# Performance work log

Hardware: AMD Instinct MI355X
Metric: run time of the kernel (lower is better)

The kernel has to match this reference:

```python
import jax, jax.numpy as jnp
import numpy as np
from jax.ops import segment_sum, segment_max

N = 100000   # nodes
E = 300000   # directed edges (3-regular fullerene cages)
F_IN = 16    # num_node_features
D = 128      # hidden_dim
H = 8        # heads
C = D // H   # per-head channels = 16
L = 4        # num_layers
G = 1600     # number of graphs in the batch
EPS = 1e-5   # BatchNorm eps
NEG_SLOPE = 0.2  # GATConv leaky_relu slope


def setup_inputs() -> dict:
    key = jax.random.key(0)
    ks = jax.random.split(key, 16)
    x = jax.random.normal(ks[0], (N, F_IN), jnp.float32)
    edge_index = jax.random.randint(ks[1], (2, E), 0, N, dtype=jnp.int64)
    batch = jnp.sort(jax.random.randint(ks[2], (N,), 0, G, dtype=jnp.int64))
    def w(k, shape, fan_in):
        return jax.random.normal(k, shape, jnp.float32) / np.sqrt(fan_in)
    return {
        "x": x, "edge_index": edge_index, "batch": batch,
        "Wp": w(ks[3], (F_IN, D), F_IN), "bp": jnp.zeros((D,), jnp.float32),
        "Wg": w(ks[4], (L, D, D), D),                       # per-layer GAT lin weight
        "asrc": w(ks[5], (L, H, C), C), "adst": w(ks[6], (L, H, C), C),
        "bg": jnp.zeros((L, D), jnp.float32),               # GAT bias
        "gamma": jnp.ones((L, D), jnp.float32), "beta": jnp.zeros((L, D), jnp.float32),
        "hW1": w(ks[7], (3, D, D // 2), D), "hb1": jnp.zeros((3, D // 2), jnp.float32),
        "hW2": w(ks[8], (3, D // 2, 1), D // 2), "hb2": jnp.zeros((3, 1), jnp.float32),
    }


def _gat_layer(x, W, att_src, att_dst, bias, src, dst):
    # PyG GATConv: linear transform per head, additive attention, scatter-softmax over dst
    xh = (x @ W).reshape(N, H, C)                      # [N,H,C]
    a_src = (xh * att_src).sum(-1)                     # [N,H]
    a_dst = (xh * att_dst).sum(-1)                     # [N,H]
    e = jax.nn.leaky_relu(a_src[src] + a_dst[dst], NEG_SLOPE)   # [E',H]
    m = segment_max(e, dst, num_segments=N)            # stable softmax per destination
    ex = jnp.exp(e - m[dst])
    denom = segment_sum(ex, dst, num_segments=N)       # > 0 (self-loops present)
    alpha = ex / denom[dst]                            # [E',H]
    out = segment_sum(alpha[:, :, None] * xh[src], dst, num_segments=N)  # [N,H,C]
    return out.reshape(N, D) + bias


def _forward(x, Wp, bp, Wg, asrc, adst, bg, gamma, beta, hW1, hb1, hW2, hb2,
             edge_index, batch):
    # add self loops (GATConv default add_self_loops=True)
    loop = jnp.arange(N, dtype=edge_index.dtype)
    src = jnp.concatenate([edge_index[0], loop])
    dst = jnp.concatenate([edge_index[1], loop])
    h = jax.nn.relu(x @ Wp + bp)
    for i in range(L):
        h = _gat_layer(h, Wg[i], asrc[i], adst[i], bg[i], src, dst)
        mu = h.mean(0)
        var = ((h - mu) ** 2).mean(0)                   # biased var (BN training math)
        h = (h - mu) / jnp.sqrt(var + EPS) * gamma[i] + beta[i]
        h = jax.nn.relu(h)                              # dropout off (eval)
    # global mean pool over graphs
    counts = segment_sum(jnp.ones((N,), h.dtype), batch, num_segments=G)
    pooled = segment_sum(h, batch, num_segments=G) / jnp.maximum(counts, 1.0)[:, None]
    # 3 output heads: Linear -> ReLU -> Linear(1)
    hid = jax.nn.relu(jnp.einsum('gd,kdm->kgm', pooled, hW1) + hb1[:, None, :])
    out = jnp.einsum('kgm,kmo->kgo', hid, hW2) + hb2[:, None, :]   # [3,G,1]
    return out[:, :, 0].T                               # [G,3]


def reference(x, edge_index, batch, Wp, bp, Wg, asrc, adst, bg, gamma, beta,
              hW1, hb1, hW2, hb2):
    return _forward(x, Wp, bp, Wg, asrc, adst, bg, gamma, beta,
                    hW1, hb1, hW2, hb2, edge_index, batch)
```

## Files before the change

kernel.cpp:

```cpp
#include <hip/hip_runtime.h>

#define D 128
#define NH 8
#define CH 16
#define NEG 0.2f
#define BN_EPS 1e-5f
#define MAXDEG 32
#define NSLICE 32
#define WROWS 144

typedef unsigned int uint;
typedef unsigned short ushort;
typedef __attribute__((ext_vector_type(8))) short bfrag;
typedef __attribute__((ext_vector_type(4))) float ffrag;

__device__ __forceinline__ float bf_lo(uint u){ return __uint_as_float(u << 16); }
__device__ __forceinline__ float bf_hi(uint u){ return __uint_as_float(u & 0xffff0000u); }
__device__ __forceinline__ float bf2f(ushort s){ return __uint_as_float(((uint)s) << 16); }
__device__ __forceinline__ ushort f2b(float f){
  uint u = __float_as_uint(f);
  u += 0x7fffu + ((u >> 16) & 1u);
  return (ushort)(u >> 16);
}

__global__ void k_scatter(const int* __restrict__ ei, int* __restrict__ deg,
                          int* __restrict__ col, int E){
  int e = blockIdx.x*blockDim.x + threadIdx.x;
  if (e < E){
    int d = ei[E + e];
    int pos = atomicAdd(&deg[d], 1);
    if (pos < MAXDEG) col[(size_t)d*MAXDEG + pos] = ei[e];
  }
}

__global__ void k_setup(const float* __restrict__ x, const float* __restrict__ Wp,
                        const float* __restrict__ bp, ushort* __restrict__ h,
                        const int* __restrict__ batch, int* __restrict__ gs,
                        const float* __restrict__ Wg, const float* __restrict__ asrc,
                        const float* __restrict__ adst, ushort* __restrict__ WtB,
                        int n, int G, int WTOT, int bInit, int bGb, int bWp){
  int bid = blockIdx.x;
  int t = threadIdx.x;
  if (bid < bInit){
    int i = bid*256 + t;
    if (i >= n*32) return;
    int nid = i >> 5, d4 = (i & 31)*4;
    const float* xr = x + nid*16;
    float s[4] = { bp[d4], bp[d4+1], bp[d4+2], bp[d4+3] };
#pragma unroll
    for (int k = 0; k < 16; k++){
      float xv = xr[k];
      const float* wr = Wp + k*D + d4;
      s[0] += xv*wr[0]; s[1] += xv*wr[1]; s[2] += xv*wr[2]; s[3] += xv*wr[3];
    }
    uint2 o;
    o.x = ((uint)f2b(fmaxf(s[0],0.f))) | (((uint)f2b(fmaxf(s[1],0.f))) << 16);
    o.y = ((uint)f2b(fmaxf(s[2],0.f))) | (((uint)f2b(fmaxf(s[3],0.f))) << 16);
    *(uint2*)(h + (size_t)nid*D + d4) = o;
  } else if (bid < bInit + bGb){
    int i = (bid - bInit)*256 + t;
    if (i >= n) return;
    int b = batch[i];
    int bpv = (i == 0) ? -1 : batch[i-1];
    for (int g = bpv + 1; g <= b; g++) gs[g] = i;
    if (i == n-1) for (int g = b + 1; g <= G; g++) gs[g] = n;
  } else if (bid < bInit + bGb + bWp){
    int i = (bid - bInit - bGb)*256 + t;
    if (i >= WTOT) return;
    int l = i >> 14, r = i & 16383, nn = r >> 7, kk = r & 127;
    WtB[(size_t)l*WROWS*D + nn*D + kk] = f2b(Wg[(size_t)l*16384 + kk*128 + nn]);
  } else {
    int i = (bid - bInit - bGb - bWp)*256 + t;
    int wscTot = (WTOT >> 14)*16*128;
    if (i >= wscTot) return;
    int l = i >> 11, r = i & 2047, j = r >> 7, k = r & 127;
    const float* wrow = Wg + (size_t)l*16384 + k*128;
    float s = 0.f;
    if (j < 8){
      const float* av = asrc + l*128 + j*16;
#pragma unroll
      for (int c = 0; c < 16; c++) s += wrow[j*16 + c] * av[c];
    } else {
      const float* av = adst + l*128 + (j - 8)*16;
#pragma unroll
      for (int c = 0; c < 16; c++) s += wrow[(j - 8)*16 + c] * av[c];
    }
    WtB[(size_t)l*WROWS*D + (128 + j)*D + k] = f2b(s);
  }
}

__global__ __launch_bounds__(512) void k_gemm(const ushort* __restrict__ hin,
                                              const ushort* __restrict__ WtB,
                                              ushort* __restrict__ xh,
                                              float* __restrict__ sc2,
                                              const float* __restrict__ bnsum,
                                              const float* __restrict__ gamma,
                                              const float* __restrict__ beta,
                                              int n, int first){
  __shared__ __align__(16) ushort wL[WROWS*136];
  __shared__ float sS[128], sB[128];
  int t = threadIdx.x;
  int wid = t >> 6, lane = t & 63, l15 = lane & 15, quad = lane >> 4;
  int n0 = blockIdx.x * 256;
  int rbase = wid*32;

  if (t < 128){
    float sc, sh;
    if (first){ sc = 1.f; sh = 0.f; }
    else {
      float s = 0.f, s2 = 0.f;
#pragma unroll 8
      for (int sl = 0; sl < NSLICE; sl++){
        s  += bnsum[sl*256 + t];
        s2 += bnsum[sl*256 + 128 + t];
      }
      float invn = 1.0f / (float)n;
      float mu = s * invn;
      float var = s2 * invn - mu*mu;
      sc = gamma[t] * rsqrtf(var + BN_EPS);
      sh = beta[t] - mu*sc;
    }
    sS[t] = sc; sB[t] = sh;
  }
#pragma unroll
  for (int i = 0; i < 5; i++){
    int u = t + i*512;
    if (u < WROWS*16){
      int r = u >> 4, c8 = u & 15;
      *(uint4*)(wL + r*136 + c8*8) = *(const uint4*)(WtB + (size_t)r*D + c8*8);
    }
  }
  __syncthreads();

  bfrag a[2][4];
#pragma unroll
  for (int mt = 0; mt < 2; mt++){
    int row = n0 + rbase + mt*16 + l15;
#pragma unroll
    for (int ks = 0; ks < 4; ks++){
      union { bfrag b; ushort us[8]; } in, ov;
      in.b = (bfrag){0,0,0,0,0,0,0,0};
      if (row < n) in.b = *(const bfrag*)(hin + (size_t)row*D + ks*32 + quad*8);
      int kb = ks*32 + quad*8;
#pragma unroll
      for (int j = 0; j < 8; j++){
        float f = bf2f(in.us[j])*sS[kb + j] + sB[kb + j];
        ov.us[j] = f2b(f > 0.f ? f : 0.f);
      }
      a[mt][ks] = ov.b;
    }
  }

  ffrag acc[2][9];
#pragma unroll
  for (int mt = 0; mt < 2; mt++)
#pragma unroll
    for (int nt = 0; nt < 9; nt++) acc[mt][nt] = (ffrag){0.f,0.f,0.f,0.f};

#pragma unroll
  for (int nt = 0; nt < 9; nt++){
#pragma unroll
    for (int ks = 0; ks < 4; ks++){
      bfrag b = *(const bfrag*)(wL + (nt*16 + l15)*136 + ks*32 + quad*8);
      acc[0][nt] = __builtin_amdgcn_mfma_f32_16x16x32_bf16(a[0][ks], b, acc[0][nt], 0, 0, 0);
      acc[1][nt] = __builtin_amdgcn_mfma_f32_16x16x32_bf16(a[1][ks], b, acc[1][nt], 0, 0, 0);
    }
  }

#pragma unroll
  for (int mt = 0; mt < 2; mt++)
#pragma unroll
    for (int r = 0; r < 4; r++){
      int grow = n0 + rbase + mt*16 + quad*4 + r;
      if (grow < n){
        sc2[(size_t)grow*16 + l15] = acc[mt][8][r];
        ushort* xr = xh + (size_t)grow*D + l15;
#pragma unroll
        for (int nt = 0; nt < 8; nt++)
          xr[nt*16] = f2b(acc[mt][nt][r]);
      }
    }
}

__global__ __launch_bounds__(512) void k_agg(const uint* __restrict__ xh32,
                                             const float* __restrict__ sc2,
                                             const int* __restrict__ deg,
                                             const int* __restrict__ col,
                                             const float* __restrict__ bg,
                                             ushort* __restrict__ hout,
                                             float* __restrict__ bnsum, int n){
  int wv = threadIdx.x >> 6;
  int l  = threadIdx.x & 63;
  int hs = l & 7;
  int jc = l >> 3;
  int n0 = (blockIdx.x*8 + wv)*2;
  int n1 = n0 + 1;
  bool vA = n0 < n, vB = n1 < n;
  int na = vA ? n0 : 0, nb = vB ? n1 : 0;

  float bnS0=0.f, bnS1=0.f, bnQ0=0.f, bnQ1=0.f;
  float b0 = bg[2*l], b1 = bg[2*l + 1];

  int cntA = deg[na]; if (cntA > MAXDEG) cntA = MAXDEG; if (!vA) cntA = 0;
  int cntB = deg[nb]; if (cntB > MAXDEG) cntB = MAXDEG; if (!vB) cntB = 0;
  const int* cbA = col + na*MAXDEG;
  const int* cbB = col + nb*MAXDEG;
  int idxA[8], idxB[8];
#pragma unroll
  for (int j = 0; j < 8; j++){ idxA[j] = cbA[j]; idxB[j] = cbB[j]; }
  int myA = cbA[jc], myB = cbB[jc];
  float asA = sc2[na*16 + hs],     asB = sc2[nb*16 + hs];
  float adA = sc2[na*16 + 8 + hs], adB = sc2[nb*16 + 8 + hs];
  uint selfA = xh32[na*64 + l],    selfB = xh32[nb*64 + l];
  float avA = sc2[myA*16 + hs],    avB = sc2[myB*16 + hs];
  uint gA[8], gB[8];
#pragma unroll
  for (int j = 0; j < 8; j++){ gA[j] = xh32[idxA[j]*64 + l]; gB[j] = xh32[idxB[j]*64 + l]; }

  int ccA = cntA < 8 ? cntA : 8;
  int ccB = cntB < 8 ? cntB : 8;
  float e0A = asA + adA; e0A = e0A > 0.f ? e0A : NEG*e0A;
  float e0B = asB + adB; e0B = e0B > 0.f ? e0B : NEG*e0B;
  float mA = e0A, dnmA = 1.f, accA0 = bf_lo(selfA), accA1 = bf_hi(selfA);
  float mB = e0B, dnmB = 1.f, accB0 = bf_lo(selfB), accB1 = bf_hi(selfB);

  float eA = -1e30f, eB = -1e30f;
  if (jc < ccA){ float ee = avA + adA; eA = ee > 0.f ? ee : NEG*ee; }
  if (jc < ccB){ float ee = avB + adB; eB = ee > 0.f ? ee : NEG*ee; }
  float mcA = eA, mcB = eB;
  mcA = fmaxf(mcA, __shfl_xor(mcA, 8));  mcB = fmaxf(mcB, __shfl_xor(mcB, 8));
  mcA = fmaxf(mcA, __shfl_xor(mcA, 16)); mcB = fmaxf(mcB, __shfl_xor(mcB, 16));
  mcA = fmaxf(mcA, __shfl_xor(mcA, 32)); mcB = fmaxf(mcB, __shfl_xor(mcB, 32));
  float mnA = fmaxf(mA, mcA),            mnB = fmaxf(mB, mcB);
  float rscA = __expf(mA - mnA),         rscB = __expf(mB - mnB);
  float wA = (jc < ccA) ? __expf(eA - mnA) : 0.f;
  float wB = (jc < ccB) ? __expf(eB - mnB) : 0.f;
  float wsA = wA, wsB = wB;
  wsA += __shfl_xor(wsA, 8);  wsB += __shfl_xor(wsB, 8);
  wsA += __shfl_xor(wsA, 16); wsB += __shfl_xor(wsB, 16);
  wsA += __shfl_xor(wsA, 32); wsB += __shfl_xor(wsB, 32);
  dnmA = dnmA*rscA + wsA;                dnmB = dnmB*rscB + wsB;
  mA = mnA;                              mB = mnB;
  float rcA = __shfl(rscA, jc),          rcB = __shfl(rscB, jc);
  accA0 *= rcA; accA1 *= rcA;            accB0 *= rcB; accB1 *= rcB;
#pragma unroll
  for (int jj = 0; jj < 8; jj++){
    float wjA = __shfl(wA, jj*8 + jc);
    float wjB = __shfl(wB, jj*8 + jc);
    accA0 += wjA * bf_lo(gA[jj]); accA1 += wjA * bf_hi(gA[jj]);
    accB0 += wjB * bf_lo(gB[jj]); accB1 += wjB * bf_hi(gB[jj]);
  }

  for (int c0 = 8; c0 < cntA; c0 += 8){
    int cc2 = cntA - c0; if (cc2 > 8) cc2 = 8;
    int my2 = cbA[c0 + jc];
    float av2 = sc2[my2*16 + hs];
    uint g2[8];
#pragma unroll
    for (int jj = 0; jj < 8; jj++) g2[jj] = xh32[cbA[c0 + jj]*64 + l];
    float e2 = -1e30f;
    if (jc < cc2){ float ee = av2 + adA; e2 = ee > 0.f ? ee : NEG*ee; }
    float mc2 = e2;
    mc2 = fmaxf(mc2, __shfl_xor(mc2, 8));
    mc2 = fmaxf(mc2, __shfl_xor(mc2, 16));
    mc2 = fmaxf(mc2, __shfl_xor(mc2, 32));
    float mn2 = fmaxf(mA, mc2);
    float rsc2 = __expf(mA - mn2);
    float w2 = (jc < cc2) ? __expf(e2 - mn2) : 0.f;
    float ws2 = w2;
    ws2 += __shfl_xor(ws2, 8);
    ws2 += __shfl_xor(ws2, 16);
    ws2 += __shfl_xor(ws2, 32);
    dnmA = dnmA*rsc2 + ws2; mA = mn2;
    float rc2 = __shfl(rsc2, jc);
    accA0 *= rc2; accA1 *= rc2;
#pragma unroll
    for (int jj = 0; jj < 8; jj++){
      float wj = __shfl(w2, jj*8 + jc);
      accA0 += wj * bf_lo(g2[jj]); accA1 += wj * bf_hi(g2[jj]);
    }
  }
  for (int c0 = 8; c0 < cntB; c0 += 8){
    int cc2 = cntB - c0; if (cc2 > 8) cc2 = 8;
    int my2 = cbB[c0 + jc];
    float av2 = sc2[my2*16 + hs];
    uint g2[8];
#pragma unroll
    for (int jj = 0; jj < 8; jj++) g2[jj] = xh32[cbB[c0 + jj]*64 + l];
    float e2 = -1e30f;
    if (jc < cc2){ float ee = av2 + adB; e2 = ee > 0.f ? ee : NEG*ee; }
    float mc2 = e2;
    mc2 = fmaxf(mc2, __shfl_xor(mc2, 8));
    mc2 = fmaxf(mc2, __shfl_xor(mc2, 16));
    mc2 = fmaxf(mc2, __shfl_xor(mc2, 32));
    float mn2 = fmaxf(mB, mc2);
    float rsc2 = __expf(mB - mn2);
    float w2 = (jc < cc2) ? __expf(e2 - mn2) : 0.f;
    float ws2 = w2;
    ws2 += __shfl_xor(ws2, 8);
    ws2 += __shfl_xor(ws2, 16);
    ws2 += __shfl_xor(ws2, 32);
    dnmB = dnmB*rsc2 + ws2; mB = mn2;
    float rc2 = __shfl(rsc2, jc);
    accB0 *= rc2; accB1 *= rc2;
#pragma unroll
    for (int jj = 0; jj < 8; jj++){
      float wj = __shfl(w2, jj*8 + jc);
      accB0 += wj * bf_lo(g2[jj]); accB1 += wj * bf_hi(g2[jj]);
    }
  }

  float dfA = __shfl(dnmA, jc), dfB = __shfl(dnmB, jc);
  float invA = 1.0f / dfA,      invB = 1.0f / dfB;
  float oA0 = accA0*invA + b0,  oA1 = accA1*invA + b1;
  float oB0 = accB0*invB + b0,  oB1 = accB1*invB + b1;
  if (vA){
    uint p = ((uint)f2b(oA0)) | (((uint)f2b(oA1)) << 16);
    ((uint*)hout)[n0*64 + l] = p;
    bnS0 += oA0; bnS1 += oA1; bnQ0 += oA0*oA0; bnQ1 += oA1*oA1;
  }
  if (vB){
    uint p = ((uint)f2b(oB0)) | (((uint)f2b(oB1)) << 16);
    ((uint*)hout)[n1*64 + l] = p;
    bnS0 += oB0; bnS1 += oB1; bnQ0 += oB0*oB0; bnQ1 += oB1*oB1;
  }

  __shared__ float red[8][64][4];
  red[wv][l][0] = bnS0; red[wv][l][1] = bnS1; red[wv][l][2] = bnQ0; red[wv][l][3] = bnQ1;
  __syncthreads();
  if (wv == 0){
    float t0 = 0.f, t1 = 0.f, t2 = 0.f, t3 = 0.f;
#pragma unroll
    for (int k = 0; k < 8; k++){
      t0 += red[k][l][0]; t1 += red[k][l][1];
      t2 += red[k][l][2]; t3 += red[k][l][3];
    }
    float* bs = bnsum + (blockIdx.x & (NSLICE - 1))*256;
    atomicAdd(&bs[2*l],       t0);
    atomicAdd(&bs[2*l + 1],   t1);
    atomicAdd(&bs[128 + 2*l], t2);
    atomicAdd(&bs[129 + 2*l], t3);
  }
}

__global__ __launch_bounds__(128) void k_poolheads(const ushort* __restrict__ h,
                                                   const int* __restrict__ gs,
                                                   const float* __restrict__ bnsum,
                                                   const float* __restrict__ gamma,
                                                   const float* __restrict__ beta,
                                                   const float* __restrict__ hW1,
                                                   const float* __restrict__ hb1,
                                                   const float* __restrict__ hW2,
                                                   const float* __restrict__ hb2,
                                                   float* __restrict__ out, int n){
  int g = blockIdx.x;
  int t = threadIdx.x;
  __shared__ float sp[128];
  int st = gs[g], en = gs[g + 1];
  float sm = 0.f, s2 = 0.f;
#pragma unroll 8
  for (int sl = 0; sl < NSLICE; sl++){
    sm += bnsum[sl*256 + t];
    s2 += bnsum[sl*256 + 128 + t];
  }
  float invn = 1.0f / (float)n;
  float mu = sm * invn;
  float var = s2 * invn - mu*mu;
  float sc = gamma[t] * rsqrtf(var + BN_EPS);
  float sh = beta[t] - mu*sc;
  float s = 0.f;
  for (int r = st; r < en; r++){
    float v = bf2f(h[(size_t)r*D + t]) * sc + sh;
    s += v > 0.f ? v : 0.f;
  }
  float cnt = (float)(en - st);
  sp[t] = s / fmaxf(cnt, 1.0f);
  __syncthreads();
  int wv = t >> 6, m = t & 63;
  for (int k = wv; k < 3; k += 2){
    float acc = hb1[k*64 + m];
    const float* w = hW1 + k*8192 + m;
#pragma unroll 16
    for (int d = 0; d < 128; d++) acc += sp[d] * w[d*64];
    float val = fmaxf(acc, 0.f) * hW2[k*64 + m];
#pragma unroll
    for (int off = 32; off; off >>= 1) val += __shfl_down(val, off);
    if (m == 0) out[(size_t)g*3 + k] = val + hb2[k];
  }
}

extern "C" void kernel_launch(void* const* d_in, const int* in_sizes, int n_in,
                              void* d_out, int out_size, void* d_ws, size_t ws_size,
                              hipStream_t stream){
  const float* x    = (const float*)d_in[0];
  const int*   ei   = (const int*)d_in[1];
  const int*   batch= (const int*)d_in[2];
  const float* Wp   = (const float*)d_in[3];
  const float* bp   = (const float*)d_in[4];
  const float* Wg   = (const float*)d_in[5];
  const float* asrc = (const float*)d_in[6];
  const float* adst = (const float*)d_in[7];
  const float* bg   = (const float*)d_in[8];
  const float* gamma= (const float*)d_in[9];
  const float* beta = (const float*)d_in[10];
  const float* hW1  = (const float*)d_in[11];
  const float* hb1  = (const float*)d_in[12];
  const float* hW2  = (const float*)d_in[13];
  const float* hb2  = (const float*)d_in[14];
  float* out = (float*)d_out;

  const int E = in_sizes[1] / 2;
  const int N = in_sizes[2];
  const int G = out_size / 3;
  const int WTOT = in_sizes[5];
  const int L = WTOT / 16384;

  char* w = (char*)d_ws;
  auto alloc = [&](size_t bytes){ char* p = w; w += (bytes + 255) & ~(size_t)255; return p; };
  ushort* h     = (ushort*)alloc((size_t)N*D*2);
  ushort* xh    = (ushort*)alloc((size_t)N*D*2);
  float* sc2    = (float*)alloc((size_t)N*16*4);
  int*   deg    = (int*)  alloc((size_t)N*4);
  int*   col    = (int*)  alloc(((size_t)N*MAXDEG + 64)*4);
  float* bnsumL = (float*)alloc((size_t)4*NSLICE*256*4);
  char*  zend   = w;
  int*   gs     = (int*)  alloc((size_t)(G + 1)*4);
  ushort* WtB   = (ushort*)alloc((size_t)L*WROWS*D*2);

  hipMemsetAsync(deg, 0, (size_t)(zend - (char*)deg), stream);
  k_scatter<<<(E + 255)/256, 256, 0, stream>>>(ei, deg, col, E);

  const int bInit = (N*32 + 255)/256;
  const int bGb   = (N + 255)/256;
  const int bWp   = (WTOT + 255)/256;
  const int bWsc  = (WTOT/8 + 255)/256;
  k_setup<<<bInit + bGb + bWp + bWsc, 256, 0, stream>>>(
      x, Wp, bp, h, batch, gs, Wg, asrc, adst, WtB,
      N, G, WTOT, bInit, bGb, bWp);

  for (int l = 0; l < 4; l++){
    float* bnPrev = bnsumL + (size_t)(l - 1)*NSLICE*256;
    float* bnCur  = bnsumL + (size_t)l*NSLICE*256;
    k_gemm<<<(N + 255)/256, 512, 0, stream>>>(h, WtB + (size_t)l*WROWS*D, xh, sc2,
                                              l == 0 ? bnCur : bnPrev,
                                              gamma + l*D, beta + l*D, N, l == 0);
    k_agg<<<(N + 15)/16, 512, 0, stream>>>((const uint*)xh, sc2, deg, col,
                                           bg + l*D, h, bnCur, N);
  }

  k_poolheads<<<G, 128, 0, stream>>>(h, gs, bnsumL + (size_t)3*NSLICE*256,
                                     gamma + 3*D, beta + 3*D,
                                     hW1, hb1, hW2, hb2, out, N);
}
```

Before: 384.8 us.

## Compute per-lane softmax in aggregation without shuffles; fuse edge scatter into setup

```diff
diff --git a/kernel.cpp b/kernel.cpp
--- a/kernel.cpp
+++ b/kernel.cpp
@@ -23,22 +23,15 @@
   return (ushort)(u >> 16);
 }
 
-__global__ void k_scatter(const int* __restrict__ ei, int* __restrict__ deg,
-                          int* __restrict__ col, int E){
-  int e = blockIdx.x*blockDim.x + threadIdx.x;
-  if (e < E){
-    int d = ei[E + e];
-    int pos = atomicAdd(&deg[d], 1);
-    if (pos < MAXDEG) col[(size_t)d*MAXDEG + pos] = ei[e];
-  }
-}
-
 __global__ void k_setup(const float* __restrict__ x, const float* __restrict__ Wp,
                         const float* __restrict__ bp, ushort* __restrict__ h,
                         const int* __restrict__ batch, int* __restrict__ gs,
                         const float* __restrict__ Wg, const float* __restrict__ asrc,
                         const float* __restrict__ adst, ushort* __restrict__ WtB,
-                        int n, int G, int WTOT, int bInit, int bGb, int bWp){
+                        const int* __restrict__ ei, int* __restrict__ deg,
+                        int* __restrict__ col,
+                        int n, int G, int WTOT, int E,
+                        int bInit, int bGb, int bWp, int bWsc){
   int bid = blockIdx.x;
   int t = threadIdx.x;
   if (bid < bInit){
@@ -69,7 +62,7 @@
     if (i >= WTOT) return;
     int l = i >> 14, r = i & 16383, nn = r >> 7, kk = r & 127;
     WtB[(size_t)l*WROWS*D + nn*D + kk] = f2b(Wg[(size_t)l*16384 + kk*128 + nn]);
-  } else {
+  } else if (bid < bInit + bGb + bWp + bWsc){
     int i = (bid - bInit - bGb - bWp)*256 + t;
     int wscTot = (WTOT >> 14)*16*128;
     if (i >= wscTot) return;
@@ -86,6 +79,13 @@
       for (int c = 0; c < 16; c++) s += wrow[(j - 8)*16 + c] * av[c];
     }
     WtB[(size_t)l*WROWS*D + (128 + j)*D + k] = f2b(s);
+  } else {
+    int e = (bid - bInit - bGb - bWp - bWsc)*256 + t;
+    if (e < E){
+      int d = ei[E + e];
+      int pos = atomicAdd(&deg[d], 1);
+      if (pos < MAXDEG) col[(size_t)d*MAXDEG + pos] = ei[e];
+    }
   }
 }
 
@@ -191,8 +191,7 @@
                                              float* __restrict__ bnsum, int n){
   int wv = threadIdx.x >> 6;
   int l  = threadIdx.x & 63;
-  int hs = l & 7;
-  int jc = l >> 3;
+  int hd = l >> 3;
   int n0 = (blockIdx.x*8 + wv)*2;
   int n1 = n0 + 1;
   bool vA = n0 < n, vB = n1 < n;
@@ -207,113 +206,107 @@
   const int* cbB = col + nb*MAXDEG;
   int idxA[8], idxB[8];
 #pragma unroll
-  for (int j = 0; j < 8; j++){ idxA[j] = cbA[j]; idxB[j] = cbB[j]; }
-  int myA = cbA[jc], myB = cbB[jc];
-  float asA = sc2[na*16 + hs],     asB = sc2[nb*16 + hs];
-  float adA = sc2[na*16 + 8 + hs], adB = sc2[nb*16 + 8 + hs];
+  for (int j = 0; j < 8; j++){
+    int ia = cbA[j]; idxA[j] = (j < cntA) ? ia : na;
+    int ib = cbB[j]; idxB[j] = (j < cntB) ? ib : nb;
+  }
+  float adA = sc2[na*16 + 8 + hd], adB = sc2[nb*16 + 8 + hd];
+  float asA = sc2[na*16 + hd],     asB = sc2[nb*16 + hd];
   uint selfA = xh32[na*64 + l],    selfB = xh32[nb*64 + l];
-  float avA = sc2[myA*16 + hs],    avB = sc2[myB*16 + hs];
+  float sA[8], sB_[8];
+#pragma unroll
+  for (int j = 0; j < 8; j++){ sA[j] = sc2[idxA[j]*16 + hd]; sB_[j] = sc2[idxB[j]*16 + hd]; }
   uint gA[8], gB[8];
 #pragma unroll
   for (int j = 0; j < 8; j++){ gA[j] = xh32[idxA[j]*64 + l]; gB[j] = xh32[idxB[j]*64 + l]; }
 
-  int ccA = cntA < 8 ? cntA : 8;
-  int ccB = cntB < 8 ? cntB : 8;
+  float eA[8], eB[8];
+#pragma unroll
+  for (int j = 0; j < 8; j++){
+    float ea = sA[j]  + adA; ea = ea > 0.f ? ea : NEG*ea;
+    float eb = sB_[j] + adB; eb = eb > 0.f ? eb : NEG*eb;
+    eA[j] = (j < cntA) ? ea : -1e30f;
+    eB[j] = (j < cntB) ? eb : -1e30f;
+  }
   float e0A = asA + adA; e0A = e0A > 0.f ? e0A : NEG*e0A;
   float e0B = asB + adB; e0B = e0B > 0.f ? e0B : NEG*e0B;
-  float mA = e0A, dnmA = 1.f, accA0 = bf_lo(selfA), accA1 = bf_hi(selfA);
-  float mB = e0B, dnmB = 1.f, accB0 = bf_lo(selfB), accB1 = bf_hi(selfB);
-
-  float eA = -1e30f, eB = -1e30f;
-  if (jc < ccA){ float ee = avA + adA; eA = ee > 0.f ? ee : NEG*ee; }
-  if (jc < ccB){ float ee = avB + adB; eB = ee > 0.f ? ee : NEG*ee; }
-  float mcA = eA, mcB = eB;
-  mcA = fmaxf(mcA, __shfl_xor(mcA, 8));  mcB = fmaxf(mcB, __shfl_xor(mcB, 8));
-  mcA = fmaxf(mcA, __shfl_xor(mcA, 16)); mcB = fmaxf(mcB, __shfl_xor(mcB, 16));
-  mcA = fmaxf(mcA, __shfl_xor(mcA, 32)); mcB = fmaxf(mcB, __shfl_xor(mcB, 32));
-  float mnA = fmaxf(mA, mcA),            mnB = fmaxf(mB, mcB);
-  float rscA = __expf(mA - mnA),         rscB = __expf(mB - mnB);
-  float wA = (jc < ccA) ? __expf(eA - mnA) : 0.f;
-  float wB = (jc < ccB) ? __expf(eB - mnB) : 0.f;
-  float wsA = wA, wsB = wB;
-  wsA += __shfl_xor(wsA, 8);  wsB += __shfl_xor(wsB, 8);
-  wsA += __shfl_xor(wsA, 16); wsB += __shfl_xor(wsB, 16);
-  wsA += __shfl_xor(wsA, 32); wsB += __shfl_xor(wsB, 32);
-  dnmA = dnmA*rscA + wsA;                dnmB = dnmB*rscB + wsB;
-  mA = mnA;                              mB = mnB;
-  float rcA = __shfl(rscA, jc),          rcB = __shfl(rscB, jc);
-  accA0 *= rcA; accA1 *= rcA;            accB0 *= rcB; accB1 *= rcB;
-#pragma unroll
-  for (int jj = 0; jj < 8; jj++){
-    float wjA = __shfl(wA, jj*8 + jc);
-    float wjB = __shfl(wB, jj*8 + jc);
-    accA0 += wjA * bf_lo(gA[jj]); accA1 += wjA * bf_hi(gA[jj]);
-    accB0 += wjB * bf_lo(gB[jj]); accB1 += wjB * bf_hi(gB[jj]);
+  float mA = fmaxf(fmaxf(fmaxf(eA[0],eA[1]), fmaxf(eA[2],eA[3])),
+                   fmaxf(fmaxf(eA[4],eA[5]), fmaxf(eA[6],eA[7])));
+  float mB = fmaxf(fmaxf(fmaxf(eB[0],eB[1]), fmaxf(eB[2],eB[3])),
+                   fmaxf(fmaxf(eB[4],eB[5]), fmaxf(eB[6],eB[7])));
+  mA = fmaxf(mA, e0A);
+  mB = fmaxf(mB, e0B);
+  float w0A = __expf(e0A - mA), w0B = __expf(e0B - mB);
+  float denA = w0A, denB = w0B;
+  float accA0 = w0A*bf_lo(selfA), accA1 = w0A*bf_hi(selfA);
+  float accB0 = w0B*bf_lo(selfB), accB1 = w0B*bf_hi(selfB);
+#pragma unroll
+  for (int j = 0; j < 8; j++){
+    float wa = __expf(eA[j] - mA);
+    float wb = __expf(eB[j] - mB);
+    denA += wa; denB += wb;
+    accA0 += wa*bf_lo(gA[j]); accA1 += wa*bf_hi(gA[j]);
+    accB0 += wb*bf_lo(gB[j]); accB1 += wb*bf_hi(gB[j]);
   }
 
   for (int c0 = 8; c0 < cntA; c0 += 8){
-    int cc2 = cntA - c0; if (cc2 > 8) cc2 = 8;
-    int my2 = cbA[c0 + jc];
-    float av2 = sc2[my2*16 + hs];
-    uint g2[8];
-#pragma unroll
-    for (int jj = 0; jj < 8; jj++) g2[jj] = xh32[cbA[c0 + jj]*64 + l];
-    float e2 = -1e30f;
-    if (jc < cc2){ float ee = av2 + adA; e2 = ee > 0.f ? ee : NEG*ee; }
-    float mc2 = e2;
-    mc2 = fmaxf(mc2, __shfl_xor(mc2, 8));
-    mc2 = fmaxf(mc2, __shfl_xor(mc2, 16));
-    mc2 = fmaxf(mc2, __shfl_xor(mc2, 32));
-    float mn2 = fmaxf(mA, mc2);
-    float rsc2 = __expf(mA - mn2);
-    float w2 = (jc < cc2) ? __expf(e2 - mn2) : 0.f;
-    float ws2 = w2;
-    ws2 += __shfl_xor(ws2, 8);
-    ws2 += __shfl_xor(ws2, 16);
-    ws2 += __shfl_xor(ws2, 32);
-    dnmA = dnmA*rsc2 + ws2; mA = mn2;
-    float rc2 = __shfl(rsc2, jc);
-    accA0 *= rc2; accA1 *= rc2;
-#pragma unroll
-    for (int jj = 0; jj < 8; jj++){
-      float wj = __shfl(w2, jj*8 + jc);
-      accA0 += wj * bf_lo(g2[jj]); accA1 += wj * bf_hi(g2[jj]);
-    }
+    int idx2[8];
+#pragma unroll
+    for (int j = 0; j < 8; j++){ int v = cbA[c0 + j]; idx2[j] = (c0 + j < cntA) ? v : na; }
+    float s2v[8]; uint g2[8];
+#pragma unroll
+    for (int j = 0; j < 8; j++) s2v[j] = sc2[idx2[j]*16 + hd];
+#pragma unroll
+    for (int j = 0; j < 8; j++) g2[j] = xh32[idx2[j]*64 + l];
+    float e2[8];
+#pragma unroll
+    for (int j = 0; j < 8; j++){
+      float ee = s2v[j] + adA; ee = ee > 0.f ? ee : NEG*ee;
+      e2[j] = (c0 + j < cntA) ? ee : -1e30f;
+    }
+    float m2 = fmaxf(fmaxf(fmaxf(e2[0],e2[1]), fmaxf(e2[2],e2[3])),
+                     fmaxf(fmaxf(e2[4],e2[5]), fmaxf(e2[6],e2[7])));
+    float mn = fmaxf(mA, m2);
+    float r = __expf(mA - mn);
+    denA *= r; accA0 *= r; accA1 *= r;
+#pragma unroll
+    for (int j = 0; j < 8; j++){
+      float w = __expf(e2[j] - mn);
+      denA += w; accA0 += w*bf_lo(g2[j]); accA1 += w*bf_hi(g2[j]);
+    }
+    mA = mn;
   }
   for (int c0 = 8; c0 < cntB; c0 += 8){
-    int cc2 = cntB - c0; if (cc2 > 8) cc2 = 8;
-    int my2 = cbB[c0 + jc];
-    float av2 = sc2[my2*16 + hs];
-    uint g2[8];
-#pragma unroll
-    for (int jj = 0; jj < 8; jj++) g2[jj] = xh32[cbB[c0 + jj]*64 + l];
-    float e2 = -1e30f;
-    if (jc < cc2){ float ee = av2 + adB; e2 = ee > 0.f ? ee : NEG*ee; }
-    float mc2 = e2;
-    mc2 = fmaxf(mc2, __shfl_xor(mc2, 8));
-    mc2 = fmaxf(mc2, __shfl_xor(mc2, 16));
-    mc2 = fmaxf(mc2, __shfl_xor(mc2, 32));
-    float mn2 = fmaxf(mB, mc2);
-    float rsc2 = __expf(mB - mn2);
-    float w2 = (jc < cc2) ? __expf(e2 - mn2) : 0.f;
-    float ws2 = w2;
-    ws2 += __shfl_xor(ws2, 8);
-    ws2 += __shfl_xor(ws2, 16);
-    ws2 += __shfl_xor(ws2, 32);
-    dnmB = dnmB*rsc2 + ws2; mB = mn2;
-    float rc2 = __shfl(rsc2, jc);
-    accB0 *= rc2; accB1 *= rc2;
-#pragma unroll
-    for (int jj = 0; jj < 8; jj++){
-      float wj = __shfl(w2, jj*8 + jc);
-      accB0 += wj * bf_lo(g2[jj]); accB1 += wj * bf_hi(g2[jj]);
-    }
-  }
-
-  float dfA = __shfl(dnmA, jc), dfB = __shfl(dnmB, jc);
-  float invA = 1.0f / dfA,      invB = 1.0f / dfB;
-  float oA0 = accA0*invA + b0,  oA1 = accA1*invA + b1;
-  float oB0 = accB0*invB + b0,  oB1 = accB1*invB + b1;
+    int idx2[8];
+#pragma unroll
+    for (int j = 0; j < 8; j++){ int v = cbB[c0 + j]; idx2[j] = (c0 + j < cntB) ? v : nb; }
+    float s2v[8]; uint g2[8];
+#pragma unroll
+    for (int j = 0; j < 8; j++) s2v[j] = sc2[idx2[j]*16 + hd];
+#pragma unroll
+    for (int j = 0; j < 8; j++) g2[j] = xh32[idx2[j]*64 + l];
+    float e2[8];
+#pragma unroll
+    for (int j = 0; j < 8; j++){
+      float ee = s2v[j] + adB; ee = ee > 0.f ? ee : NEG*ee;
+      e2[j] = (c0 + j < cntB) ? ee : -1e30f;
+    }
+    float m2 = fmaxf(fmaxf(fmaxf(e2[0],e2[1]), fmaxf(e2[2],e2[3])),
+                     fmaxf(fmaxf(e2[4],e2[5]), fmaxf(e2[6],e2[7])));
+    float mn = fmaxf(mB, m2);
+    float r = __expf(mB - mn);
+    denB *= r; accB0 *= r; accB1 *= r;
+#pragma unroll
+    for (int j = 0; j < 8; j++){
+      float w = __expf(e2[j] - mn);
+      denB += w; accB0 += w*bf_lo(g2[j]); accB1 += w*bf_hi(g2[j]);
+    }
+    mB = mn;
+  }
+
+  float invA = 1.0f / denA, invB = 1.0f / denB;
+  float oA0 = accA0*invA + b0, oA1 = accA1*invA + b1;
+  float oB0 = accB0*invB + b0, oB1 = accB1*invB + b1;
   if (vA){
     uint p = ((uint)f2b(oA0)) | (((uint)f2b(oA1)) << 16);
     ((uint*)hout)[n0*64 + l] = p;
@@ -421,22 +414,22 @@
   ushort* xh    = (ushort*)alloc((size_t)N*D*2);
   float* sc2    = (float*)alloc((size_t)N*16*4);
   int*   deg    = (int*)  alloc((size_t)N*4);
-  int*   col    = (int*)  alloc(((size_t)N*MAXDEG + 64)*4);
   float* bnsumL = (float*)alloc((size_t)4*NSLICE*256*4);
   char*  zend   = w;
+  int*   col    = (int*)  alloc(((size_t)N*MAXDEG + 64)*4);
   int*   gs     = (int*)  alloc((size_t)(G + 1)*4);
   ushort* WtB   = (ushort*)alloc((size_t)L*WROWS*D*2);
 
   hipMemsetAsync(deg, 0, (size_t)(zend - (char*)deg), stream);
-  k_scatter<<<(E + 255)/256, 256, 0, stream>>>(ei, deg, col, E);
 
   const int bInit = (N*32 + 255)/256;
   const int bGb   = (N + 255)/256;
   const int bWp   = (WTOT + 255)/256;
   const int bWsc  = (WTOT/8 + 255)/256;
-  k_setup<<<bInit + bGb + bWp + bWsc, 256, 0, stream>>>(
+  const int bSc   = (E + 255)/256;
+  k_setup<<<bInit + bGb + bWp + bWsc + bSc, 256, 0, stream>>>(
       x, Wp, bp, h, batch, gs, Wg, asrc, adst, WtB,
-      N, G, WTOT, bInit, bGb, bWp);
+      ei, deg, col, N, G, WTOT, E, bInit, bGb, bWp, bWsc);
 
   for (int l = 0; l < 4; l++){
     float* bnPrev = bnsumL + (size_t)(l - 1)*NSLICE*256;
```

New measurement: 413.4 us. +7.4%, slower.

## Skip zeroing col array and register-block input projection over four nodes

Applied to the files above, without the earlier changes.

```diff
diff --git a/kernel.cpp b/kernel.cpp
--- a/kernel.cpp
+++ b/kernel.cpp
@@ -13,6 +13,7 @@
 typedef unsigned short ushort;
 typedef __attribute__((ext_vector_type(8))) short bfrag;
 typedef __attribute__((ext_vector_type(4))) float ffrag;
+typedef __attribute__((ext_vector_type(16))) float fvec16;
 
 __device__ __forceinline__ float bf_lo(uint u){ return __uint_as_float(u << 16); }
 __device__ __forceinline__ float bf_hi(uint u){ return __uint_as_float(u & 0xffff0000u); }
@@ -43,20 +44,40 @@
   int t = threadIdx.x;
   if (bid < bInit){
     int i = bid*256 + t;
-    if (i >= n*32) return;
-    int nid = i >> 5, d4 = (i & 31)*4;
-    const float* xr = x + nid*16;
-    float s[4] = { bp[d4], bp[d4+1], bp[d4+2], bp[d4+3] };
+    int g4 = i >> 5, d4 = (i & 31)*4;
+    int base = g4*4;
+    if (base >= n) return;
+    fvec16 xr[4];
+#pragma unroll
+    for (int m = 0; m < 4; m++){
+      int node = base + m; if (node >= n) node = n - 1;
+      xr[m] = *(const fvec16*)(x + (size_t)node*16);
+    }
+    float s[4][4];
+#pragma unroll
+    for (int m = 0; m < 4; m++){
+      s[m][0] = bp[d4]; s[m][1] = bp[d4+1]; s[m][2] = bp[d4+2]; s[m][3] = bp[d4+3];
+    }
 #pragma unroll
     for (int k = 0; k < 16; k++){
-      float xv = xr[k];
       const float* wr = Wp + k*D + d4;
-      s[0] += xv*wr[0]; s[1] += xv*wr[1]; s[2] += xv*wr[2]; s[3] += xv*wr[3];
-    }
-    uint2 o;
-    o.x = ((uint)f2b(fmaxf(s[0],0.f))) | (((uint)f2b(fmaxf(s[1],0.f))) << 16);
-    o.y = ((uint)f2b(fmaxf(s[2],0.f))) | (((uint)f2b(fmaxf(s[3],0.f))) << 16);
-    *(uint2*)(h + (size_t)nid*D + d4) = o;
+      float w0 = wr[0], w1 = wr[1], w2 = wr[2], w3 = wr[3];
+#pragma unroll
+      for (int m = 0; m < 4; m++){
+        float xv = xr[m][k];
+        s[m][0] += xv*w0; s[m][1] += xv*w1; s[m][2] += xv*w2; s[m][3] += xv*w3;
+      }
+    }
+#pragma unroll
+    for (int m = 0; m < 4; m++){
+      int node = base + m;
+      if (node < n){
+        uint2 o;
+        o.x = ((uint)f2b(fmaxf(s[m][0],0.f))) | (((uint)f2b(fmaxf(s[m][1],0.f))) << 16);
+        o.y = ((uint)f2b(fmaxf(s[m][2],0.f))) | (((uint)f2b(fmaxf(s[m][3],0.f))) << 16);
+        *(uint2*)(h + (size_t)node*D + d4) = o;
+      }
+    }
   } else if (bid < bInit + bGb){
     int i = (bid - bInit)*256 + t;
     if (i >= n) return;
@@ -207,8 +228,12 @@
   const int* cbB = col + nb*MAXDEG;
   int idxA[8], idxB[8];
 #pragma unroll
-  for (int j = 0; j < 8; j++){ idxA[j] = cbA[j]; idxB[j] = cbB[j]; }
-  int myA = cbA[jc], myB = cbB[jc];
+  for (int j = 0; j < 8; j++){
+    int ia = cbA[j]; idxA[j] = (j < cntA) ? ia : na;
+    int ib = cbB[j]; idxB[j] = (j < cntB) ? ib : nb;
+  }
+  int myA = cbA[jc]; myA = (jc < cntA) ? myA : na;
+  int myB = cbB[jc]; myB = (jc < cntB) ? myB : nb;
   float asA = sc2[na*16 + hs],     asB = sc2[nb*16 + hs];
   float adA = sc2[na*16 + 8 + hs], adB = sc2[nb*16 + 8 + hs];
   uint selfA = xh32[na*64 + l],    selfB = xh32[nb*64 + l];
@@ -253,11 +278,14 @@
 
   for (int c0 = 8; c0 < cntA; c0 += 8){
     int cc2 = cntA - c0; if (cc2 > 8) cc2 = 8;
-    int my2 = cbA[c0 + jc];
+    int my2 = cbA[c0 + jc]; my2 = (c0 + jc < cntA) ? my2 : na;
     float av2 = sc2[my2*16 + hs];
     uint g2[8];
 #pragma unroll
-    for (int jj = 0; jj < 8; jj++) g2[jj] = xh32[cbA[c0 + jj]*64 + l];
+    for (int jj = 0; jj < 8; jj++){
+      int v = cbA[c0 + jj]; v = (c0 + jj < cntA) ? v : na;
+      g2[jj] = xh32[v*64 + l];
+    }
     float e2 = -1e30f;
     if (jc < cc2){ float ee = av2 + adA; e2 = ee > 0.f ? ee : NEG*ee; }
     float mc2 = e2;
@@ -282,11 +310,14 @@
   }
   for (int c0 = 8; c0 < cntB; c0 += 8){
     int cc2 = cntB - c0; if (cc2 > 8) cc2 = 8;
-    int my2 = cbB[c0 + jc];
+    int my2 = cbB[c0 + jc]; my2 = (c0 + jc < cntB) ? my2 : nb;
     float av2 = sc2[my2*16 + hs];
     uint g2[8];
 #pragma unroll
-    for (int jj = 0; jj < 8; jj++) g2[jj] = xh32[cbB[c0 + jj]*64 + l];
+    for (int jj = 0; jj < 8; jj++){
+      int v = cbB[c0 + jj]; v = (c0 + jj < cntB) ? v : nb;
+      g2[jj] = xh32[v*64 + l];
+    }
     float e2 = -1e30f;
     if (jc < cc2){ float ee = av2 + adB; e2 = ee > 0.f ? ee : NEG*ee; }
     float mc2 = e2;
@@ -421,16 +452,16 @@
   ushort* xh    = (ushort*)alloc((size_t)N*D*2);
   float* sc2    = (float*)alloc((size_t)N*16*4);
   int*   deg    = (int*)  alloc((size_t)N*4);
-  int*   col    = (int*)  alloc(((size_t)N*MAXDEG + 64)*4);
   float* bnsumL = (float*)alloc((size_t)4*NSLICE*256*4);
   char*  zend   = w;
+  int*   col    = (int*)  alloc(((size_t)N*MAXDEG + 64)*4);
   int*   gs     = (int*)  alloc((size_t)(G + 1)*4);
   ushort* WtB   = (ushort*)alloc((size_t)L*WROWS*D*2);
 
   hipMemsetAsync(deg, 0, (size_t)(zend - (char*)deg), stream);
   k_scatter<<<(E + 255)/256, 256, 0, stream>>>(ei, deg, col, E);
 
-  const int bInit = (N*32 + 255)/256;
+  const int bInit = (((N + 3)/4)*32 + 255)/256;
   const int bGb   = (N + 255)/256;
   const int bWp   = (WTOT + 255)/256;
   const int bWsc  = (WTOT/8 + 255)/256;
```

Measured after the change: 441.0 us. 1.15x slower.

## Halve GEMM rows per block and stop zeroing the padded adjacency buffer

Applied to the files above, without the earlier changes.

```diff
diff --git a/kernel.cpp b/kernel.cpp
--- a/kernel.cpp
+++ b/kernel.cpp
@@ -101,8 +101,8 @@
   __shared__ float sS[128], sB[128];
   int t = threadIdx.x;
   int wid = t >> 6, lane = t & 63, l15 = lane & 15, quad = lane >> 4;
-  int n0 = blockIdx.x * 256;
-  int rbase = wid*32;
+  int n0 = blockIdx.x * 128;
+  int rbase = wid*16;
 
   if (t < 128){
     float sc, sh;
@@ -132,54 +132,46 @@
   }
   __syncthreads();
 
-  bfrag a[2][4];
-#pragma unroll
-  for (int mt = 0; mt < 2; mt++){
-    int row = n0 + rbase + mt*16 + l15;
-#pragma unroll
-    for (int ks = 0; ks < 4; ks++){
-      union { bfrag b; ushort us[8]; } in, ov;
-      in.b = (bfrag){0,0,0,0,0,0,0,0};
-      if (row < n) in.b = *(const bfrag*)(hin + (size_t)row*D + ks*32 + quad*8);
-      int kb = ks*32 + quad*8;
-#pragma unroll
-      for (int j = 0; j < 8; j++){
-        float f = bf2f(in.us[j])*sS[kb + j] + sB[kb + j];
-        ov.us[j] = f2b(f > 0.f ? f : 0.f);
-      }
-      a[mt][ks] = ov.b;
-    }
-  }
-
-  ffrag acc[2][9];
-#pragma unroll
-  for (int mt = 0; mt < 2; mt++)
-#pragma unroll
-    for (int nt = 0; nt < 9; nt++) acc[mt][nt] = (ffrag){0.f,0.f,0.f,0.f};
+  bfrag a[4];
+  int arow = n0 + rbase + l15;
+#pragma unroll
+  for (int ks = 0; ks < 4; ks++){
+    union { bfrag b; ushort us[8]; } in, ov;
+    in.b = (bfrag){0,0,0,0,0,0,0,0};
+    if (arow < n) in.b = *(const bfrag*)(hin + (size_t)arow*D + ks*32 + quad*8);
+    int kb = ks*32 + quad*8;
+#pragma unroll
+    for (int j = 0; j < 8; j++){
+      float f = bf2f(in.us[j])*sS[kb + j] + sB[kb + j];
+      ov.us[j] = f2b(f > 0.f ? f : 0.f);
+    }
+    a[ks] = ov.b;
+  }
+
+  ffrag acc[9];
+#pragma unroll
+  for (int nt = 0; nt < 9; nt++) acc[nt] = (ffrag){0.f,0.f,0.f,0.f};
 
 #pragma unroll
   for (int nt = 0; nt < 9; nt++){
 #pragma unroll
     for (int ks = 0; ks < 4; ks++){
       bfrag b = *(const bfrag*)(wL + (nt*16 + l15)*136 + ks*32 + quad*8);
-      acc[0][nt] = __builtin_amdgcn_mfma_f32_16x16x32_bf16(a[0][ks], b, acc[0][nt], 0, 0, 0);
-      acc[1][nt] = __builtin_amdgcn_mfma_f32_16x16x32_bf16(a[1][ks], b, acc[1][nt], 0, 0, 0);
-    }
-  }
-
-#pragma unroll
-  for (int mt = 0; mt < 2; mt++)
-#pragma unroll
-    for (int r = 0; r < 4; r++){
-      int grow = n0 + rbase + mt*16 + quad*4 + r;
-      if (grow < n){
-        sc2[(size_t)grow*16 + l15] = acc[mt][8][r];
-        ushort* xr = xh + (size_t)grow*D + l15;
-#pragma unroll
-        for (int nt = 0; nt < 8; nt++)
-          xr[nt*16] = f2b(acc[mt][nt][r]);
-      }
-    }
+      acc[nt] = __builtin_amdgcn_mfma_f32_16x16x32_bf16(a[ks], b, acc[nt], 0, 0, 0);
+    }
+  }
+
+#pragma unroll
+  for (int r = 0; r < 4; r++){
+    int grow = n0 + rbase + quad*4 + r;
+    if (grow < n){
+      sc2[(size_t)grow*16 + l15] = acc[8][r];
+      ushort* xr = xh + (size_t)grow*D + l15;
+#pragma unroll
+      for (int nt = 0; nt < 8; nt++)
+        xr[nt*16] = f2b(acc[nt][r]);
+    }
+  }
 }
 
 __global__ __launch_bounds__(512) void k_agg(const uint* __restrict__ xh32,
@@ -207,8 +199,12 @@
   const int* cbB = col + nb*MAXDEG;
   int idxA[8], idxB[8];
 #pragma unroll
-  for (int j = 0; j < 8; j++){ idxA[j] = cbA[j]; idxB[j] = cbB[j]; }
-  int myA = cbA[jc], myB = cbB[jc];
+  for (int j = 0; j < 8; j++){
+    int ia = cbA[j]; idxA[j] = (j < cntA) ? ia : na;
+    int ib = cbB[j]; idxB[j] = (j < cntB) ? ib : nb;
+  }
+  int myA = cbA[jc]; myA = (jc < cntA) ? myA : na;
+  int myB = cbB[jc]; myB = (jc < cntB) ? myB : nb;
   float asA = sc2[na*16 + hs],     asB = sc2[nb*16 + hs];
   float adA = sc2[na*16 + 8 + hs], adB = sc2[nb*16 + 8 + hs];
   uint selfA = xh32[na*64 + l],    selfB = xh32[nb*64 + l];
@@ -253,11 +249,14 @@
 
   for (int c0 = 8; c0 < cntA; c0 += 8){
     int cc2 = cntA - c0; if (cc2 > 8) cc2 = 8;
-    int my2 = cbA[c0 + jc];
+    int my2 = cbA[c0 + jc]; my2 = (c0 + jc < cntA) ? my2 : na;
     float av2 = sc2[my2*16 + hs];
     uint g2[8];
 #pragma unroll
-    for (int jj = 0; jj < 8; jj++) g2[jj] = xh32[cbA[c0 + jj]*64 + l];
+    for (int jj = 0; jj < 8; jj++){
+      int v = cbA[c0 + jj]; v = (c0 + jj < cntA) ? v : na;
+      g2[jj] = xh32[v*64 + l];
+    }
     float e2 = -1e30f;
     if (jc < cc2){ float ee = av2 + adA; e2 = ee > 0.f ? ee : NEG*ee; }
     float mc2 = e2;
@@ -282,11 +281,14 @@
   }
   for (int c0 = 8; c0 < cntB; c0 += 8){
     int cc2 = cntB - c0; if (cc2 > 8) cc2 = 8;
-    int my2 = cbB[c0 + jc];
+    int my2 = cbB[c0 + jc]; my2 = (c0 + jc < cntB) ? my2 : nb;
     float av2 = sc2[my2*16 + hs];
     uint g2[8];
 #pragma unroll
-    for (int jj = 0; jj < 8; jj++) g2[jj] = xh32[cbB[c0 + jj]*64 + l];
+    for (int jj = 0; jj < 8; jj++){
+      int v = cbB[c0 + jj]; v = (c0 + jj < cntB) ? v : nb;
+      g2[jj] = xh32[v*64 + l];
+    }
     float e2 = -1e30f;
     if (jc < cc2){ float ee = av2 + adB; e2 = ee > 0.f ? ee : NEG*ee; }
     float mc2 = e2;
@@ -421,9 +423,9 @@
   ushort* xh    = (ushort*)alloc((size_t)N*D*2);
   float* sc2    = (float*)alloc((size_t)N*16*4);
   int*   deg    = (int*)  alloc((size_t)N*4);
-  int*   col    = (int*)  alloc(((size_t)N*MAXDEG + 64)*4);
   float* bnsumL = (float*)alloc((size_t)4*NSLICE*256*4);
   char*  zend   = w;
+  int*   col    = (int*)  alloc(((size_t)N*MAXDEG + 64)*4);
   int*   gs     = (int*)  alloc((size_t)(G + 1)*4);
   ushort* WtB   = (ushort*)alloc((size_t)L*WROWS*D*2);
 
@@ -441,7 +443,7 @@
   for (int l = 0; l < 4; l++){
     float* bnPrev = bnsumL + (size_t)(l - 1)*NSLICE*256;
     float* bnCur  = bnsumL + (size_t)l*NSLICE*256;
-    k_gemm<<<(N + 255)/256, 512, 0, stream>>>(h, WtB + (size_t)l*WROWS*D, xh, sc2,
+    k_gemm<<<(N + 127)/128, 512, 0, stream>>>(h, WtB + (size_t)l*WROWS*D, xh, sc2,
                                               l == 0 ? bnCur : bnPrev,
                                               gamma + l*D, beta + l*D, N, l == 0);
     k_agg<<<(N + 15)/16, 512, 0, stream>>>((const uint*)xh, sc2, deg, col,
```

New measurement: 410.9 us. +6.8%, slower.
